# Kernel optimization log

Measured on AMD Instinct MI355X. Metric: run time of the kernel, lower is better.

The kernel has to match this reference:

```python
import jax, jax.numpy as jnp
import numpy as np
from jax.ops import segment_sum, segment_max

N = 38332
E = 1200000
C = 64
POI_LEN = 38333
CAT_LEN = 400
LAYERS = 5


def _glorot(key, shape):
    fan_in, fan_out = shape[0], shape[-1]
    lim = float(np.sqrt(6.0 / (fan_in + fan_out)))
    return jax.random.uniform(key, shape, jnp.float32, -lim, lim)


def gcn_conv(x, src, dst, ew, W, b):
    # PyG GCNConv: x@W, add self-loops (weight 1), symmetric norm, scatter-sum at dst
    h = x @ W  # [N, Cout]
    ar = jnp.arange(N, dtype=src.dtype)
    s = jnp.concatenate([src, ar])
    d = jnp.concatenate([dst, ar])
    w = jnp.concatenate([ew, jnp.ones((N,), ew.dtype)])
    deg = segment_sum(w, d, num_segments=N)
    dinv = jnp.where(deg > 0, jax.lax.rsqrt(jnp.maximum(deg, 1e-12)), 0.0)
    norm = dinv[s] * w * dinv[d]
    out = segment_sum(h[s] * norm[:, None], d, num_segments=N)
    return out + b


def graph_norm(x, w, b, alpha, eps=1e-5):
    mean = jnp.mean(x, axis=0, keepdims=True)
    out = x - alpha * mean
    var = jnp.mean(out * out, axis=0, keepdims=True)
    return out * jax.lax.rsqrt(var + eps) * w + b


def gat_conv(x, src, dst, W, att_src, att_dst, b):
    # PyG GATConv, heads=1, add_self_loops=True, negative_slope=0.2
    h = x @ W  # [N, C]
    ar = jnp.arange(N, dtype=src.dtype)
    s = jnp.concatenate([src, ar])
    d = jnp.concatenate([dst, ar])
    a_s = h @ att_src  # [N]
    a_d = h @ att_dst
    e = jax.nn.leaky_relu(a_s[s] + a_d[d], 0.2)  # [E+N]
    m = segment_max(e, d, num_segments=N)
    ex = jnp.exp(e - m[d])
    z = segment_sum(ex, d, num_segments=N)
    alpha = ex / (z[d] + 1e-16)
    out = segment_sum(h[s] * alpha[:, None], d, num_segments=N)
    return out + b


def setup_inputs() -> dict:
    key = jax.random.key(0)
    ks = jax.random.split(key, 32)
    inp = {
        'poi_idx': jax.random.randint(ks[0], (N,), 0, POI_LEN, jnp.int32),
        'cat_idx': jax.random.randint(ks[1], (N,), 0, CAT_LEN, jnp.int32),
        'feat': jax.random.normal(ks[2], (N, 3), jnp.float32),
        'edge_index': jax.random.randint(ks[3], (2, E), 0, N, jnp.int32),
        'weight': jax.random.uniform(ks[4], (E,), jnp.float32),
        'poi_emb': jax.random.normal(ks[5], (POI_LEN, 300), jnp.float32),
        'cat_emb': jax.random.normal(ks[6], (CAT_LEN, 100), jnp.float32),
        'W_in': _glorot(ks[7], (403, C)),
        'b_in': jnp.zeros((C,), jnp.float32),
        'gcn_W': jax.vmap(lambda k: _glorot(k, (C, C)))(jax.random.split(ks[8], LAYERS)),
        'gcn_b': jnp.zeros((LAYERS, C), jnp.float32),
        'gn_w': jnp.ones((LAYERS, C), jnp.float32),
        'gn_b': jnp.zeros((LAYERS, C), jnp.float32),
        'gn_a': jnp.ones((LAYERS, C), jnp.float32),
        'gat_W': jax.vmap(lambda k: _glorot(k, (C, C)))(jax.random.split(ks[9], LAYERS)),
        'gat_att_src': jax.random.normal(ks[10], (LAYERS, C), jnp.float32) * 0.1,
        'gat_att_dst': jax.random.normal(ks[11], (LAYERS, C), jnp.float32) * 0.1,
        'gat_b': jnp.zeros((LAYERS, C), jnp.float32),
        'W_out': _glorot(ks[12], (C, 1)),
        'b_out': jnp.zeros((1,), jnp.float32),
        'fc1_W': _glorot(ks[13], (N, 128)),
        'fc1_b': jnp.zeros((128,), jnp.float32),
        'fc2_W': _glorot(ks[14], (128, POI_LEN)),
        'fc2_b': jnp.zeros((POI_LEN,), jnp.float32),
    }
    return inp


def reference(poi_idx, cat_idx, feat, edge_index, weight, poi_emb, cat_emb,
              W_in, b_in, gcn_W, gcn_b, gn_w, gn_b, gn_a,
              gat_W, gat_att_src, gat_att_dst, gat_b,
              W_out, b_out, fc1_W, fc1_b, fc2_W, fc2_b):
    src, dst = edge_index[0], edge_index[1]
    lrelu = lambda v: jax.nn.leaky_relu(v, 0.01)  # nn.LeakyReLU default
    x = jnp.concatenate([poi_emb[poi_idx], cat_emb[cat_idx], feat], axis=1)  # [N,403]
    x = lrelu(gcn_conv(x, src, dst, weight, W_in, b_in))  # [N,64]
    for i in range(LAYERS):
        t = gcn_conv(x, src, dst, weight, gcn_W[i], gcn_b[i])
        t = lrelu(graph_norm(t, gn_w[i], gn_b[i], gn_a[i]))
        x = x + t
        t = gat_conv(x, src, dst, gat_W[i], gat_att_src[i], gat_att_dst[i], gat_b[i])
        t = lrelu(graph_norm(t, gn_w[i], gn_b[i], gn_a[i]))
        x = x + t
    x = lrelu(gcn_conv(x, src, dst, weight, W_out, b_out)).reshape(-1)  # [N]
    h = jax.nn.relu(x @ fc1_W + fc1_b)
    out = jax.nn.relu(h @ fc2_W + fc2_b)  # [POI_LEN]
    return out
```

## Files before the change

kernel.cpp:

```cpp
#include <hip/hip_runtime.h>
#include <hip/hip_fp16.h>

#define NN 38332
#define NE 1200000
#define POI 38333
#define NWG 192
#define CHUNK (NE/NWG)
#define SBLK 256
#define FBLK 1024

__device__ __forceinline__ float lrelu01(float v){ return v > 0.f ? v : 0.01f*v; }

__device__ __forceinline__ void load8(const __half* h, int s, int c8, float* f){
  uint4 q = *(const uint4*)((const __half*)h + (size_t)s*64 + c8);
  __half2 h0 = *(__half2*)&q.x, h1 = *(__half2*)&q.y, h2 = *(__half2*)&q.z, h3 = *(__half2*)&q.w;
  float2 r0 = __half22float2(h0), r1 = __half22float2(h1), r2 = __half22float2(h2), r3 = __half22float2(h3);
  f[0]=r0.x; f[1]=r0.y; f[2]=r1.x; f[3]=r1.y; f[4]=r2.x; f[5]=r2.y; f[6]=r3.x; f[7]=r3.y;
}
__device__ __forceinline__ void load8(const float* h, int s, int c8, float* f){
  float4 a = *(const float4*)(h + (size_t)s*64 + c8);
  float4 b = *(const float4*)(h + (size_t)s*64 + c8 + 4);
  f[0]=a.x; f[1]=a.y; f[2]=a.z; f[3]=a.w; f[4]=b.x; f[5]=b.y; f[6]=b.z; f[7]=b.w;
}
__device__ __forceinline__ void store8(float* out, int n, int cb, const float* o){
  *(float4*)&out[(size_t)n*64 + cb]     = make_float4(o[0],o[1],o[2],o[3]);
  *(float4*)&out[(size_t)n*64 + cb + 4] = make_float4(o[4],o[5],o[6],o[7]);
}
__device__ __forceinline__ void store8(__half* out, int n, int cb, const float* o){
  __half2 q0 = __floats2half2_rn(o[0], o[1]);
  __half2 q1 = __floats2half2_rn(o[2], o[3]);
  __half2 q2 = __floats2half2_rn(o[4], o[5]);
  __half2 q3 = __floats2half2_rn(o[6], o[7]);
  uint4 q;
  q.x = *(unsigned*)&q0; q.y = *(unsigned*)&q1; q.z = *(unsigned*)&q2; q.w = *(unsigned*)&q3;
  *(uint4*)((__half*)out + (size_t)n*64 + cb) = q;
}

__global__ __launch_bounds__(1024) void k_hist(const int* __restrict__ dst,
                                               int* __restrict__ partial){
  __shared__ int hist[NN];
  for (int i = threadIdx.x; i < NN; i += 1024) hist[i] = 0;
  __syncthreads();
  int base = blockIdx.x*CHUNK;
  for (int k = threadIdx.x; k < CHUNK; k += 1024)
    atomicAdd(&hist[dst[base + k]], 1);
  __syncthreads();
  for (int i = threadIdx.x; i < NN; i += 1024)
    partial[(size_t)blockIdx.x*NN + i] = hist[i];
}

__global__ __launch_bounds__(256) void k_b1(int* __restrict__ partial, int* __restrict__ counts){
  int bin = blockIdx.x*256 + threadIdx.x;
  if (bin < NN){
    int run = 0;
    for (int wg = 0; wg < NWG; ++wg){
      int v = partial[(size_t)wg*NN + bin];
      partial[(size_t)wg*NN + bin] = run;
      run += v;
    }
    counts[bin] = run;
  }
}

__global__ __launch_bounds__(1024) void k_scan(const int* __restrict__ counts, int* rowptr){
  __shared__ int part[1024];
  int tid = threadIdx.x;
  const int per = (NN + 1023)/1024;
  int base = tid*per;
  int s = 0;
  for (int k = 0; k < per; k++){ int i = base + k; if (i < NN) s += counts[i]; }
  part[tid] = s;
  __syncthreads();
  for (int off = 1; off < 1024; off <<= 1){
    int v = (tid >= off) ? part[tid-off] : 0;
    __syncthreads();
    part[tid] += v;
    __syncthreads();
  }
  int run = (tid == 0) ? 0 : part[tid-1];
  for (int k = 0; k < per; k++){
    int i = base + k;
    if (i < NN){ rowptr[i] = run; run += counts[i]; }
  }
  if (tid == 1023) rowptr[NN] = run;
}

__global__ __launch_bounds__(1024) void k_scatter(const int* __restrict__ src,
                                                  const int* __restrict__ dst,
                                                  const float* __restrict__ ew,
                                                  const int* __restrict__ rowptr,
                                                  const int* __restrict__ partial,
                                                  int2* __restrict__ cw){
  __shared__ int cur[NN];
  for (int i = threadIdx.x; i < NN; i += 1024)
    cur[i] = rowptr[i] + partial[(size_t)blockIdx.x*NN + i];
  __syncthreads();
  int base = blockIdx.x*CHUNK;
  for (int k = threadIdx.x; k < CHUNK; k += 1024){
    int e = base + k;
    int d = dst[e];
    int pos = atomicAdd(&cur[d], 1);
    cw[pos] = make_int2(src[e], __float_as_int(ew[e]));
  }
}

__global__ __launch_bounds__(256) void k_dinv(const int* __restrict__ rowptr,
                                              const int2* __restrict__ cw,
                                              float* __restrict__ dinv){
  int lane = threadIdx.x & 63;
  int n = blockIdx.x*4 + (threadIdx.x >> 6);
  int beg = rowptr[n], end = rowptr[n+1];
  float s = 0.f;
  for (int e = beg + lane; e < end; e += 64) s += __int_as_float(cw[e].y);
  #pragma unroll
  for (int off = 32; off; off >>= 1) s += __shfl_xor(s, off);
  if (lane == 0) dinv[n] = rsqrtf(1.0f + s);
}

__global__ __launch_bounds__(256) void k_scale(const int* __restrict__ rowptr,
                                               const float* __restrict__ dinv,
                                               int2* __restrict__ cw){
  int lane = threadIdx.x & 63;
  int n = blockIdx.x*4 + (threadIdx.x >> 6);
  float dn = dinv[n];
  int beg = rowptr[n], end = rowptr[n+1];
  for (int e = beg + lane; e < end; e += 64){
    int2 p = cw[e];
    cw[e].y = __float_as_int(dinv[p.x]*__int_as_float(p.y)*dn);
  }
}

template<int K>
__global__ __launch_bounds__(256) void k_proj(const float* __restrict__ emb,
                                              const float* __restrict__ W,
                                              float* __restrict__ outp, int rows){
  int lane = threadIdx.x & 63;
  int base = __builtin_amdgcn_readfirstlane(blockIdx.x*16 + (threadIdx.x >> 6)*4);
  float acc[4] = {0.f,0.f,0.f,0.f};
  constexpr int NCH = (K + 63)/64;
  #pragma unroll
  for (int ch = 0; ch < NCH; ++ch){
    float Wreg[64];
    #pragma unroll
    for (int j = 0; j < 64; ++j)
      Wreg[j] = (ch*64 + j < K) ? W[(ch*64 + j)*64 + lane] : 0.f;
    #pragma unroll
    for (int r = 0; r < 4; ++r){
      int row = base + r;
      if (row < rows){
        const float* er = emb + (size_t)row*K + ch*64;
        #pragma unroll
        for (int j = 0; j < 64; ++j)
          if (ch*64 + j < K) acc[r] = fmaf(er[j], Wreg[j], acc[r]);
      }
    }
  }
  #pragma unroll
  for (int r = 0; r < 4; ++r){
    int row = base + r;
    if (row < rows) outp[(size_t)row*64 + lane] = acc[r];
  }
}

__global__ __launch_bounds__(256) void k_gather(const int* __restrict__ poi_idx,
                                                const int* __restrict__ cat_idx,
                                                const float* __restrict__ feat,
                                                const float* __restrict__ pproj,
                                                const float* __restrict__ cproj,
                                                const float* __restrict__ Wf,
                                                __half* __restrict__ outh){
  int i = blockIdx.x*256 + threadIdx.x;
  int n = i >> 6, c = i & 63;
  float f0 = feat[n*3], f1 = feat[n*3+1], f2 = feat[n*3+2];
  float v = pproj[(size_t)poi_idx[n]*64 + c] + cproj[(size_t)cat_idx[n]*64 + c];
  v = fmaf(f0, Wf[c], v);
  v = fmaf(f1, Wf[64 + c], v);
  v = fmaf(f2, Wf[128 + c], v);
  outh[i] = __float2half(v);
}

template<bool ATT, bool RESID>
__global__ __launch_bounds__(256) void k_lin64f(float* __restrict__ x,
                                                const __half* __restrict__ t,
                                                const float* __restrict__ stats,
                                                const float* __restrict__ gb,
                                                const float* __restrict__ W,
                                                const float* __restrict__ att_src,
                                                const float* __restrict__ att_dst,
                                                __half* __restrict__ h,
                                                float* __restrict__ a_s,
                                                float* __restrict__ a_d){
  int lane = threadIdx.x & 63;
  int base = blockIdx.x*32 + (threadIdx.x >> 6)*8;
  float Wreg[64];
  #pragma unroll
  for (int j = 0; j < 64; ++j) Wreg[j] = W[j*64 + lane];
  float coef = 0.f, shift = 0.f, gbv = 0.f;
  if (RESID){
    coef  = stats[128 + lane];
    shift = stats[192 + lane];
    gbv   = gb[lane];
  }
  float as_l = 0.f, ad_l = 0.f;
  if (ATT){ as_l = att_src[lane]; ad_l = att_dst[lane]; }
  #pragma unroll
  for (int r = 0; r < 8; ++r){
    int row = base + r;
    if (row < NN){
      float xn = x[(size_t)row*64 + lane];
      if (RESID){
        float tv = __half2float(t[(size_t)row*64 + lane]);
        xn += lrelu01((tv - shift)*coef + gbv);
        x[(size_t)row*64 + lane] = xn;
      }
      int xi = __float_as_int(xn);
      float acc = 0.f;
      #pragma unroll
      for (int j = 0; j < 64; ++j)
        acc = fmaf(__int_as_float(__builtin_amdgcn_readlane(xi, j)), Wreg[j], acc);
      h[(size_t)row*64 + lane] = __float2half(acc);
      if (ATT){
        float s1 = acc*as_l, s2 = acc*ad_l;
        #pragma unroll
        for (int off = 32; off; off >>= 1){ s1 += __shfl_xor(s1, off); s2 += __shfl_xor(s2, off); }
        if (lane == 0){ a_s[row] = s1; a_d[row] = s2; }
      }
    }
  }
}

template<bool DO_LRELU, typename TIN, typename TOUT>
__global__ __launch_bounds__(256) void k_gcn_prop(const TIN* __restrict__ h,
                                                  const int* __restrict__ rowptr,
                                                  const int2* __restrict__ cw,
                                                  const float* __restrict__ dinv,
                                                  const float* __restrict__ bias,
                                                  TOUT* __restrict__ out){
  int lane = threadIdx.x & 63;
  int n = __builtin_amdgcn_readfirstlane(blockIdx.x*4 + (threadIdx.x >> 6));
  int beg = rowptr[n], end = rowptr[n+1];
  int deg = end - beg;
  int g  = lane >> 3;
  int c8 = (lane & 7) << 3;
  float acc[8] = {0.f,0.f,0.f,0.f,0.f,0.f,0.f,0.f};
  float acc2[8] = {0.f,0.f,0.f,0.f,0.f,0.f,0.f,0.f};
  if (deg < 64){
    int sv = n; float wv = 0.f;
    if (lane < deg){
      int2 p = cw[beg + lane];
      sv = p.x; wv = __int_as_float(p.y);
    } else if (lane == deg){
      float di = dinv[n];
      wv = di*di;
    }
    int ne = deg + 1;
    int nit = (ne + 15) >> 4;
    float wA0 = __shfl(wv, g),     wB0 = __shfl(wv, 8 + g);
    int   sA0 = __shfl(sv, g),     sB0 = __shfl(sv, 8 + g);
    float fA0[8], fB0[8];
    load8(h, sA0, c8, fA0); load8(h, sB0, c8, fB0);
    for (int it = 1; it < nit; ++it){
      int eiA = (it << 4) + g, eiB = eiA + 8;
      float wA1 = __shfl(wv, eiA), wB1 = __shfl(wv, eiB);
      int   sA1 = __shfl(sv, eiA), sB1 = __shfl(sv, eiB);
      float fA1[8], fB1[8];
      load8(h, sA1, c8, fA1); load8(h, sB1, c8, fB1);
      #pragma unroll
      for (int j = 0; j < 8; ++j){
        acc[j]  = fmaf(wA0, fA0[j], acc[j]);
        acc2[j] = fmaf(wB0, fB0[j], acc2[j]);
      }
      wA0 = wA1; wB0 = wB1;
      #pragma unroll
      for (int j = 0; j < 8; ++j){ fA0[j] = fA1[j]; fB0[j] = fB1[j]; }
    }
    #pragma unroll
    for (int j = 0; j < 8; ++j){
      acc[j]  = fmaf(wA0, fA0[j], acc[j]);
      acc2[j] = fmaf(wB0, fB0[j], acc2[j]);
    }
  } else {
    {
      float di = dinv[n];
      float w = (g == 0) ? di*di : 0.f;
      float f[8]; load8(h, n, c8, f);
      #pragma unroll
      for (int j = 0; j < 8; ++j) acc[j] = fmaf(w, f[j], acc[j]);
    }
    int nit = (deg + 7) >> 3;
    for (int it = 0; it < nit; ++it){
      int ei = (it << 3) + g;
      int2 p = cw[beg + (ei < deg ? ei : 0)];
      float w = (ei < deg) ? __int_as_float(p.y) : 0.f;
      float f[8]; load8(h, p.x, c8, f);
      #pragma unroll
      for (int j = 0; j < 8; ++j) acc[j] = fmaf(w, f[j], acc[j]);
    }
  }
  #pragma unroll
  for (int j = 0; j < 8; ++j) acc[j] += acc2[j];
  #pragma unroll
  for (int m = 8; m < 64; m <<= 1){
    #pragma unroll
    for (int j = 0; j < 8; ++j) acc[j] += __shfl_xor(acc[j], m);
  }
  if (lane < 8){
    int cb = lane << 3;
    float4 b0 = *(const float4*)&bias[cb];
    float4 b1 = *(const float4*)&bias[cb + 4];
    float o[8] = {acc[0]+b0.x, acc[1]+b0.y, acc[2]+b0.z, acc[3]+b0.w,
                  acc[4]+b1.x, acc[5]+b1.y, acc[6]+b1.z, acc[7]+b1.w};
    if (DO_LRELU){
      #pragma unroll
      for (int j = 0; j < 8; ++j) o[j] = lrelu01(o[j]);
    }
    store8(out, n, cb, o);
  }
}

__global__ __launch_bounds__(256) void k_gat_prop(const __half* __restrict__ h,
                                                  const int* __restrict__ rowptr,
                                                  const int2* __restrict__ cw,
                                                  const float* __restrict__ a_s,
                                                  const float* __restrict__ a_d,
                                                  const float* __restrict__ bias,
                                                  __half* __restrict__ out){
  int lane = threadIdx.x & 63;
  int n = __builtin_amdgcn_readfirstlane(blockIdx.x*4 + (threadIdx.x >> 6));
  int beg = rowptr[n], end = rowptr[n+1];
  int deg = end - beg;
  float ad = a_d[n];
  float se = a_s[n] + ad; se = se > 0.f ? se : 0.2f*se;
  if (deg <= 64){
    int s = 0; float v = -1e30f;
    if (lane < deg){
      s = cw[beg + lane].x;
      v = a_s[s] + ad; v = v > 0.f ? v : 0.2f*v;
    }
    float m = fmaxf(se, v);
    #pragma unroll
    for (int off = 32; off; off >>= 1) m = fmaxf(m, __shfl_xor(m, off));
    float ev = (lane < deg) ? __expf(v - m) : 0.f;
    float z = ev;
    #pragma unroll
    for (int off = 32; off; off >>= 1) z += __shfl_xor(z, off);
    float es = __expf(se - m);
    z += es;
    float zinv = 1.0f/(z + 1e-16f);
    int g = lane >> 3, c8 = (lane & 7) << 3;
    float acc[8] = {0.f,0.f,0.f,0.f,0.f,0.f,0.f,0.f};
    float acc2[8] = {0.f,0.f,0.f,0.f,0.f,0.f,0.f,0.f};
    { float f[8]; load8(h, n, c8, f);
      float w = (g == 0) ? es : 0.f;
      #pragma unroll
      for (int j = 0; j < 8; ++j) acc[j] = fmaf(w, f[j], acc[j]);
    }
    int nit = (deg + 15) >> 4;
    if (nit > 0){
      float wA0 = __shfl(ev, g),     wB0 = __shfl(ev, 8 + g);
      int   sA0 = __shfl(s,  g),     sB0 = __shfl(s,  8 + g);
      float fA0[8], fB0[8];
      load8(h, sA0, c8, fA0); load8(h, sB0, c8, fB0);
      for (int it = 1; it < nit; ++it){
        int eiA = (it << 4) + g, eiB = eiA + 8;
        float wA1 = __shfl(ev, eiA), wB1 = __shfl(ev, eiB);
        int   sA1 = __shfl(s,  eiA), sB1 = __shfl(s,  eiB);
        float fA1[8], fB1[8];
        load8(h, sA1, c8, fA1); load8(h, sB1, c8, fB1);
        #pragma unroll
        for (int j = 0; j < 8; ++j){
          acc[j]  = fmaf(wA0, fA0[j], acc[j]);
          acc2[j] = fmaf(wB0, fB0[j], acc2[j]);
        }
        wA0 = wA1; wB0 = wB1;
        #pragma unroll
        for (int j = 0; j < 8; ++j){ fA0[j] = fA1[j]; fB0[j] = fB1[j]; }
      }
      #pragma unroll
      for (int j = 0; j < 8; ++j){
        acc[j]  = fmaf(wA0, fA0[j], acc[j]);
        acc2[j] = fmaf(wB0, fB0[j], acc2[j]);
      }
    }
    #pragma unroll
    for (int j = 0; j < 8; ++j) acc[j] += acc2[j];
    #pragma unroll
    for (int mm = 8; mm < 64; mm <<= 1){
      #pragma unroll
      for (int j = 0; j < 8; ++j) acc[j] += __shfl_xor(acc[j], mm);
    }
    if (lane < 8){
      int cb = lane << 3;
      float4 b0 = *(const float4*)&bias[cb];
      float4 b1 = *(const float4*)&bias[cb + 4];
      float o[8] = {fmaf(acc[0],zinv,b0.x), fmaf(acc[1],zinv,b0.y), fmaf(acc[2],zinv,b0.z), fmaf(acc[3],zinv,b0.w),
                    fmaf(acc[4],zinv,b1.x), fmaf(acc[5],zinv,b1.y), fmaf(acc[6],zinv,b1.z), fmaf(acc[7],zinv,b1.w)};
      store8(out, n, cb, o);
    }
  } else {
    float m = se;
    for (int e = beg + lane; e < end; e += 64){
      float v = a_s[cw[e].x] + ad; v = v > 0.f ? v : 0.2f*v;
      m = fmaxf(m, v);
    }
    #pragma unroll
    for (int off = 32; off; off >>= 1) m = fmaxf(m, __shfl_xor(m, off));
    float z = 0.f;
    for (int e = beg + lane; e < end; e += 64){
      float v = a_s[cw[e].x] + ad; v = v > 0.f ? v : 0.2f*v;
      z += __expf(v - m);
    }
    #pragma unroll
    for (int off = 32; off; off >>= 1) z += __shfl_xor(z, off);
    float es = __expf(se - m);
    z += es;
    float zinv = 1.0f/(z + 1e-16f);
    float acc = es*(float)h[(size_t)n*64 + lane];
    for (int e = beg; e < end; ++e){
      int sj = cw[e].x;
      float v = a_s[sj] + ad; v = v > 0.f ? v : 0.2f*v;
      acc = fmaf(__expf(v - m), (float)h[(size_t)sj*64 + lane], acc);
    }
    out[(size_t)n*64 + lane] = __float2half(acc*zinv + bias[lane]);
  }
}

__global__ __launch_bounds__(256) void k_colstats(const __half* __restrict__ t,
                                                  float* __restrict__ pstats){
  int c4  = (threadIdx.x & 15)*4;
  int sub = threadIdx.x >> 4;
  float s0=0.f,s1=0.f,s2=0.f,s3=0.f, q0=0.f,q1=0.f,q2=0.f,q3=0.f;
  for (int n = blockIdx.x*16 + sub; n < NN; n += gridDim.x*16){
    uint2 u = *(const uint2*)((const __half*)t + (size_t)n*64 + c4);
    __half2 h0 = *(__half2*)&u.x, h1 = *(__half2*)&u.y;
    float2 r0 = __half22float2(h0), r1 = __half22float2(h1);
    s0 += r0.x; q0 = fmaf(r0.x, r0.x, q0);
    s1 += r0.y; q1 = fmaf(r0.y, r0.y, q1);
    s2 += r1.x; q2 = fmaf(r1.x, r1.x, q2);
    s3 += r1.y; q3 = fmaf(r1.y, r1.y, q3);
  }
  __shared__ float ls[256][4], ls2[256][4];
  ls[threadIdx.x][0]=s0; ls[threadIdx.x][1]=s1; ls[threadIdx.x][2]=s2; ls[threadIdx.x][3]=s3;
  ls2[threadIdx.x][0]=q0; ls2[threadIdx.x][1]=q1; ls2[threadIdx.x][2]=q2; ls2[threadIdx.x][3]=q3;
  __syncthreads();
  if (threadIdx.x < 16){
    int cg = threadIdx.x;
    float a0=0.f,a1=0.f,a2=0.f,a3=0.f, b0=0.f,b1=0.f,b2=0.f,b3=0.f;
    #pragma unroll
    for (int k = 0; k < 16; ++k){
      int idx = k*16 + cg;
      a0 += ls[idx][0]; a1 += ls[idx][1]; a2 += ls[idx][2]; a3 += ls[idx][3];
      b0 += ls2[idx][0]; b1 += ls2[idx][1]; b2 += ls2[idx][2]; b3 += ls2[idx][3];
    }
    int cb = cg*4;
    pstats[blockIdx.x*128 + cb    ] = a0;
    pstats[blockIdx.x*128 + cb + 1] = a1;
    pstats[blockIdx.x*128 + cb + 2] = a2;
    pstats[blockIdx.x*128 + cb + 3] = a3;
    pstats[blockIdx.x*128 + 64 + cb    ] = b0;
    pstats[blockIdx.x*128 + 64 + cb + 1] = b1;
    pstats[blockIdx.x*128 + 64 + cb + 2] = b2;
    pstats[blockIdx.x*128 + 64 + cb + 3] = b3;
  }
}

__global__ __launch_bounds__(256) void k_chan(const float* __restrict__ pstats,
                                              const float* __restrict__ gw,
                                              const float* __restrict__ ga,
                                              float* __restrict__ stats){
  int lane = threadIdx.x & 63, w = threadIdx.x >> 6;
  float s = 0.f, s2 = 0.f;
  for (int blk = w*(SBLK/4); blk < (w+1)*(SBLK/4); ++blk){
    s  += pstats[blk*128 + lane];
    s2 += pstats[blk*128 + 64 + lane];
  }
  __shared__ float ls[256], ls2[256];
  ls[threadIdx.x] = s; ls2[threadIdx.x] = s2;
  __syncthreads();
  if (threadIdx.x < 64){
    int c = threadIdx.x;
    s  = ls[c]  + ls[c+64]  + ls[c+128]  + ls[c+192];
    s2 = ls2[c] + ls2[c+64] + ls2[c+128] + ls2[c+192];
    const float invN = 1.0f/(float)NN;
    float m  = s*invN, ms = s2*invN, a = ga[c];
    float var = ms - m*m*a*(2.0f - a);
    stats[128 + c] = rsqrtf(var + 1e-5f)*gw[c];
    stats[192 + c] = a*m;
  }
}

__global__ __launch_bounds__(256) void k_outlinf(const float* __restrict__ x,
                                                 const __half* __restrict__ t,
                                                 const float* __restrict__ stats,
                                                 const float* __restrict__ gb,
                                                 const float* __restrict__ Wout,
                                                 float* __restrict__ h1){
  int lane = threadIdx.x & 63, wave = threadIdx.x >> 6;
  int n = blockIdx.x*4 + wave;
  float coef  = stats[128 + lane];
  float shift = stats[192 + lane];
  float xn = x[(size_t)n*64 + lane];
  float tv = __half2float(t[(size_t)n*64 + lane]);
  xn += lrelu01((tv - shift)*coef + gb[lane]);
  float v = xn*Wout[lane];
  #pragma unroll
  for (int off = 32; off; off >>= 1) v += __shfl_xor(v, off);
  if (lane == 0) h1[n] = v;
}

__global__ __launch_bounds__(256) void k_prop1(const float* __restrict__ h1,
                                               const int* __restrict__ rowptr,
                                               const int2* __restrict__ cw,
                                               const float* __restrict__ dinv,
                                               const float* __restrict__ b_out,
                                               float* __restrict__ xs){
  int lane = threadIdx.x & 63;
  int n = blockIdx.x*32 + (threadIdx.x >> 6)*8 + (lane >> 3);
  bool ok = n < NN;
  int beg = ok ? rowptr[n] : 0;
  int end = ok ? rowptr[n+1] : 0;
  float acc = 0.f;
  for (int e = beg + (lane & 7); e < end; e += 8){
    int2 p = cw[e];
    acc = fmaf(__int_as_float(p.y), h1[p.x], acc);
  }
  acc += __shfl_xor(acc, 1);
  acc += __shfl_xor(acc, 2);
  acc += __shfl_xor(acc, 4);
  if (ok && (lane & 7) == 0){
    float di = dinv[n];
    xs[n] = lrelu01(acc + di*di*h1[n] + b_out[0]);
  }
}

__global__ __launch_bounds__(256) void k_fc1(const float* __restrict__ xs,
                                             const float* __restrict__ W,
                                             float* __restrict__ pfc){
  int j = threadIdx.x & 127, half = threadIdx.x >> 7;
  float acc = 0.f;
  for (int n = blockIdx.x*2 + half; n < NN; n += gridDim.x*2)
    acc = fmaf(xs[n], W[(size_t)n*128 + j], acc);
  __shared__ float ls[256];
  ls[threadIdx.x] = acc;
  __syncthreads();
  if (threadIdx.x < 128) pfc[blockIdx.x*128 + j] = ls[j] + ls[128 + j];
}

__global__ __launch_bounds__(256) void k_fcr(const float* __restrict__ pfc,
                                             const float* __restrict__ fc1_b,
                                             float* __restrict__ hfc){
  int j = blockIdx.x;
  int tid = threadIdx.x;
  float acc = 0.f;
  #pragma unroll
  for (int k = 0; k < FBLK/256; ++k)
    acc += pfc[(size_t)(tid + k*256)*128 + j];
  __shared__ float ls[256];
  ls[tid] = acc;
  __syncthreads();
  for (int off = 128; off > 0; off >>= 1){
    if (tid < off) ls[tid] += ls[tid + off];
    __syncthreads();
  }
  if (tid == 0){
    float v = ls[0] + fc1_b[j];
    hfc[j] = v > 0.f ? v : 0.f;
  }
}

__global__ __launch_bounds__(256) void k_fc2(const float* __restrict__ hfc,
                                             const float* __restrict__ W2,
                                             const float* __restrict__ b2,
                                             float* __restrict__ out){
  __shared__ float hs[128];
  if (threadIdx.x < 128) hs[threadIdx.x] = hfc[threadIdx.x];
  __syncthreads();
  int p = blockIdx.x*64 + (threadIdx.x >> 2);
  int q = threadIdx.x & 3;
  if (p < POI){
    float acc = 0.f;
    #pragma unroll
    for (int j = q; j < 128; j += 4)
      acc = fmaf(hs[j], W2[(size_t)j*POI + p], acc);
    acc += __shfl_xor(acc, 1);
    acc += __shfl_xor(acc, 2);
    if (q == 0){
      float v = acc + b2[p];
      out[p] = v > 0.f ? v : 0.f;
    }
  }
}

extern "C" void kernel_launch(void* const* d_in, const int* in_sizes, int n_in,
                              void* d_out, int out_size, void* d_ws, size_t ws_size,
                              hipStream_t stream) {
  const int*   poi_idx = (const int*)d_in[0];
  const int*   cat_idx = (const int*)d_in[1];
  const float* feat    = (const float*)d_in[2];
  const int*   eidx    = (const int*)d_in[3];
  const int*   src     = eidx;
  const int*   dst     = eidx + NE;
  const float* ew      = (const float*)d_in[4];
  const float* poi_emb = (const float*)d_in[5];
  const float* cat_emb = (const float*)d_in[6];
  const float* W_in    = (const float*)d_in[7];
  const float* b_in    = (const float*)d_in[8];
  const float* gcn_W   = (const float*)d_in[9];
  const float* gcn_b   = (const float*)d_in[10];
  const float* gn_w    = (const float*)d_in[11];
  const float* gn_b    = (const float*)d_in[12];
  const float* gn_a    = (const float*)d_in[13];
  const float* gat_W   = (const float*)d_in[14];
  const float* att_s   = (const float*)d_in[15];
  const float* att_d   = (const float*)d_in[16];
  const float* gat_b   = (const float*)d_in[17];
  const float* W_out   = (const float*)d_in[18];
  const float* b_out   = (const float*)d_in[19];
  const float* fc1_W   = (const float*)d_in[20];
  const float* fc1_b   = (const float*)d_in[21];
  const float* fc2_W   = (const float*)d_in[22];
  const float* fc2_b   = (const float*)d_in[23];
  float* out = (float*)d_out;

  char* p = (char*)d_ws;
  auto alloc = [&](size_t bytes){ void* r = (void*)p; p += (bytes + 255) & ~(size_t)255; return r; };
  float*  x      = (float*) alloc((size_t)NN*64*4);
  __half* t      = (__half*)alloc((size_t)NN*64*2);
  __half* h      = (__half*)alloc((size_t)NN*64*2);
  int*    partial= (int*)   alloc((size_t)NWG*NN*4);
  float*  pproj  = (float*) partial;
  float*  cproj  = (float*) alloc((size_t)400*64*4);
  int2*   cw     = (int2*)  alloc((size_t)NE*8);
  float*  dinv   = (float*) alloc(NN*4);
  int*    counts = (int*)   alloc(NN*4);
  int*    rowptr = (int*)   alloc((NN+1)*4);
  float*  a_s    = (float*) alloc(NN*4);
  float*  a_d    = (float*) alloc(NN*4);
  float*  pstats = (float*) alloc((size_t)SBLK*128*4);
  float*  stats  = (float*) alloc(256*4);
  float*  h1     = (float*) alloc(NN*4);
  float*  xs     = (float*) alloc(NN*4);
  float*  pfc    = (float*) alloc((size_t)FBLK*128*4);
  float*  hfc    = (float*) alloc(128*4);

  const int G_N   = (NN + 255)/256;
  const int G_W4  = NN/4;
  const int G_L   = (NN + 31)/32;
  const int G_PJ  = (POI + 15)/16;
  const int G_EL  = NN*64/256;
  const int G_P1  = (NN + 31)/32;
  const int G_F2  = (POI + 63)/64;

  k_hist   <<<NWG, 1024, 0, stream>>>(dst, partial);
  k_b1     <<<G_N, 256, 0, stream>>>(partial, counts);
  k_scan   <<<1, 1024, 0, stream>>>(counts, rowptr);
  k_scatter<<<NWG, 1024, 0, stream>>>(src, dst, ew, rowptr, partial, cw);
  k_dinv   <<<G_W4, 256, 0, stream>>>(rowptr, cw, dinv);
  k_scale  <<<G_W4, 256, 0, stream>>>(rowptr, dinv, cw);

  k_proj<300><<<G_PJ, 256, 0, stream>>>(poi_emb, W_in, pproj, POI);
  k_proj<100><<<25, 256, 0, stream>>>(cat_emb, W_in + 300*64, cproj, 400);
  k_gather<<<G_EL, 256, 0, stream>>>(poi_idx, cat_idx, feat, pproj, cproj, W_in + 400*64, t);
  k_gcn_prop<true, __half, float><<<G_W4, 256, 0, stream>>>(t, rowptr, cw, dinv, b_in, x);

  for (int i = 0; i < 5; i++){
    if (i == 0)
      k_lin64f<false,false><<<G_L, 256, 0, stream>>>(x, nullptr, nullptr, nullptr,
                                                     gcn_W, nullptr, nullptr, h, nullptr, nullptr);
    else
      k_lin64f<false,true><<<G_L, 256, 0, stream>>>(x, t, stats, gn_b + (i-1)*64,
                                                    gcn_W + i*4096, nullptr, nullptr, h, nullptr, nullptr);
    k_gcn_prop<false, __half, __half><<<G_W4, 256, 0, stream>>>(h, rowptr, cw, dinv, gcn_b + i*64, t);
    k_colstats<<<SBLK, 256, 0, stream>>>(t, pstats);
    k_chan<<<1, 256, 0, stream>>>(pstats, gn_w + i*64, gn_a + i*64, stats);
    k_lin64f<true,true><<<G_L, 256, 0, stream>>>(x, t, stats, gn_b + i*64,
                                                 gat_W + i*4096, att_s + i*64, att_d + i*64, h, a_s, a_d);
    k_gat_prop<<<G_W4, 256, 0, stream>>>(h, rowptr, cw, a_s, a_d, gat_b + i*64, t);
    k_colstats<<<SBLK, 256, 0, stream>>>(t, pstats);
    k_chan<<<1, 256, 0, stream>>>(pstats, gn_w + i*64, gn_a + i*64, stats);
  }

  k_outlinf<<<G_W4, 256, 0, stream>>>(x, t, stats, gn_b + 4*64, W_out, h1);
  k_prop1<<<G_P1, 256, 0, stream>>>(h1, rowptr, cw, dinv, b_out, xs);
  k_fc1<<<FBLK, 256, 0, stream>>>(xs, fc1_W, pfc);
  k_fcr<<<128, 256, 0, stream>>>(pfc, fc1_b, hfc);
  k_fc2<<<G_F2, 256, 0, stream>>>(hfc, fc2_W, fc2_b, out);
}
```

Before: 896.1 us.

## Split propagation kernels across channel halves and shrink histogram partials to 16-bit

The GCN and GAT propagation kernels now launch twice as many blocks, and each wave handles one 32-channel half of a node. This gives 16 edges in flight per iteration, and the short-degree path becomes a fixed 2–4 gather step with no loop. The per-workgroup histogram partials are stored as unsigned short, halving that buffer's traffic in the CSR build. The trade-off is that the edge indices, softmax weights and attention logits for each node are loaded and computed twice. The 16-bit partials are safe only while per-bin counts stay below 65536.

```diff
diff --git a/kernel.cpp b/kernel.cpp
--- a/kernel.cpp
+++ b/kernel.cpp
@@ -37,7 +37,7 @@
 }
 
 __global__ __launch_bounds__(1024) void k_hist(const int* __restrict__ dst,
-                                               int* __restrict__ partial){
+                                               unsigned short* __restrict__ partial){
   __shared__ int hist[NN];
   for (int i = threadIdx.x; i < NN; i += 1024) hist[i] = 0;
   __syncthreads();
@@ -46,16 +46,17 @@
     atomicAdd(&hist[dst[base + k]], 1);
   __syncthreads();
   for (int i = threadIdx.x; i < NN; i += 1024)
-    partial[(size_t)blockIdx.x*NN + i] = hist[i];
-}
-
-__global__ __launch_bounds__(256) void k_b1(int* __restrict__ partial, int* __restrict__ counts){
+    partial[(size_t)blockIdx.x*NN + i] = (unsigned short)hist[i];
+}
+
+__global__ __launch_bounds__(256) void k_b1(unsigned short* __restrict__ partial,
+                                            int* __restrict__ counts){
   int bin = blockIdx.x*256 + threadIdx.x;
   if (bin < NN){
     int run = 0;
     for (int wg = 0; wg < NWG; ++wg){
       int v = partial[(size_t)wg*NN + bin];
-      partial[(size_t)wg*NN + bin] = run;
+      partial[(size_t)wg*NN + bin] = (unsigned short)run;
       run += v;
     }
     counts[bin] = run;
@@ -89,11 +90,11 @@
                                                   const int* __restrict__ dst,
                                                   const float* __restrict__ ew,
                                                   const int* __restrict__ rowptr,
-                                                  const int* __restrict__ partial,
+                                                  const unsigned short* __restrict__ partial,
                                                   int2* __restrict__ cw){
   __shared__ int cur[NN];
   for (int i = threadIdx.x; i < NN; i += 1024)
-    cur[i] = rowptr[i] + partial[(size_t)blockIdx.x*NN + i];
+    cur[i] = rowptr[i] + (int)partial[(size_t)blockIdx.x*NN + i];
   __syncthreads();
   int base = blockIdx.x*CHUNK;
   for (int k = threadIdx.x; k < CHUNK; k += 1024){
@@ -237,13 +238,13 @@
                                                   const float* __restrict__ bias,
                                                   TOUT* __restrict__ out){
   int lane = threadIdx.x & 63;
-  int n = __builtin_amdgcn_readfirstlane(blockIdx.x*4 + (threadIdx.x >> 6));
+  int half = blockIdx.x & 1;
+  int n = __builtin_amdgcn_readfirstlane((blockIdx.x >> 1)*4 + (threadIdx.x >> 6));
   int beg = rowptr[n], end = rowptr[n+1];
   int deg = end - beg;
-  int g  = lane >> 3;
-  int c8 = (lane & 7) << 3;
+  int g  = lane >> 2;
+  int co = half*32 + (lane & 3)*8;
   float acc[8] = {0.f,0.f,0.f,0.f,0.f,0.f,0.f,0.f};
-  float acc2[8] = {0.f,0.f,0.f,0.f,0.f,0.f,0.f,0.f};
   if (deg < 64){
     int sv = n; float wv = 0.f;
     if (lane < deg){
@@ -254,58 +255,51 @@
       wv = di*di;
     }
     int ne = deg + 1;
-    int nit = (ne + 15) >> 4;
-    float wA0 = __shfl(wv, g),     wB0 = __shfl(wv, 8 + g);
-    int   sA0 = __shfl(sv, g),     sB0 = __shfl(sv, 8 + g);
-    float fA0[8], fB0[8];
-    load8(h, sA0, c8, fA0); load8(h, sB0, c8, fB0);
-    for (int it = 1; it < nit; ++it){
-      int eiA = (it << 4) + g, eiB = eiA + 8;
-      float wA1 = __shfl(wv, eiA), wB1 = __shfl(wv, eiB);
-      int   sA1 = __shfl(sv, eiA), sB1 = __shfl(sv, eiB);
-      float fA1[8], fB1[8];
-      load8(h, sA1, c8, fA1); load8(h, sB1, c8, fB1);
+    float w0 = __shfl(wv, g),      w1 = __shfl(wv, 16 + g);
+    int   s0 = __shfl(sv, g),      s1 = __shfl(sv, 16 + g);
+    float f0[8], f1[8];
+    load8(h, s0, co, f0); load8(h, s1, co, f1);
+    if (ne > 32){
+      float w2 = __shfl(wv, 32 + g), w3 = __shfl(wv, 48 + g);
+      int   s2 = __shfl(sv, 32 + g), s3 = __shfl(sv, 48 + g);
+      float f2[8], f3[8];
+      load8(h, s2, co, f2); load8(h, s3, co, f3);
       #pragma unroll
       for (int j = 0; j < 8; ++j){
-        acc[j]  = fmaf(wA0, fA0[j], acc[j]);
-        acc2[j] = fmaf(wB0, fB0[j], acc2[j]);
+        acc[j] = fmaf(w2, f2[j], acc[j]);
+        acc[j] = fmaf(w3, f3[j], acc[j]);
       }
-      wA0 = wA1; wB0 = wB1;
-      #pragma unroll
-      for (int j = 0; j < 8; ++j){ fA0[j] = fA1[j]; fB0[j] = fB1[j]; }
     }
     #pragma unroll
     for (int j = 0; j < 8; ++j){
-      acc[j]  = fmaf(wA0, fA0[j], acc[j]);
-      acc2[j] = fmaf(wB0, fB0[j], acc2[j]);
+      acc[j] = fmaf(w0, f0[j], acc[j]);
+      acc[j] = fmaf(w1, f1[j], acc[j]);
     }
   } else {
     {
       float di = dinv[n];
       float w = (g == 0) ? di*di : 0.f;
-      float f[8]; load8(h, n, c8, f);
+      float f[8]; load8(h, n, co, f);
       #pragma unroll
       for (int j = 0; j < 8; ++j) acc[j] = fmaf(w, f[j], acc[j]);
     }
-    int nit = (deg + 7) >> 3;
+    int nit = (deg + 15) >> 4;
     for (int it = 0; it < nit; ++it){
-      int ei = (it << 3) + g;
+      int ei = (it << 4) + g;
       int2 p = cw[beg + (ei < deg ? ei : 0)];
       float w = (ei < deg) ? __int_as_float(p.y) : 0.f;
-      float f[8]; load8(h, p.x, c8, f);
+      float f[8]; load8(h, p.x, co, f);
       #pragma unroll
       for (int j = 0; j < 8; ++j) acc[j] = fmaf(w, f[j], acc[j]);
     }
   }
   #pragma unroll
-  for (int j = 0; j < 8; ++j) acc[j] += acc2[j];
-  #pragma unroll
-  for (int m = 8; m < 64; m <<= 1){
+  for (int m = 4; m < 64; m <<= 1){
     #pragma unroll
     for (int j = 0; j < 8; ++j) acc[j] += __shfl_xor(acc[j], m);
   }
-  if (lane < 8){
-    int cb = lane << 3;
+  if (lane < 4){
+    int cb = half*32 + lane*8;
     float4 b0 = *(const float4*)&bias[cb];
     float4 b1 = *(const float4*)&bias[cb + 4];
     float o[8] = {acc[0]+b0.x, acc[1]+b0.y, acc[2]+b0.z, acc[3]+b0.w,
@@ -326,71 +320,59 @@
                                                   const float* __restrict__ bias,
                                                   __half* __restrict__ out){
   int lane = threadIdx.x & 63;
-  int n = __builtin_amdgcn_readfirstlane(blockIdx.x*4 + (threadIdx.x >> 6));
+  int half = blockIdx.x & 1;
+  int n = __builtin_amdgcn_readfirstlane((blockIdx.x >> 1)*4 + (threadIdx.x >> 6));
   int beg = rowptr[n], end = rowptr[n+1];
   int deg = end - beg;
   float ad = a_d[n];
   float se = a_s[n] + ad; se = se > 0.f ? se : 0.2f*se;
-  if (deg <= 64){
-    int s = 0; float v = -1e30f;
+  if (deg < 64){
+    int s = n; float v = -1e30f;
     if (lane < deg){
       s = cw[beg + lane].x;
       v = a_s[s] + ad; v = v > 0.f ? v : 0.2f*v;
-    }
-    float m = fmaxf(se, v);
+    } else if (lane == deg){
+      v = se;
+    }
+    float m = v;
     #pragma unroll
     for (int off = 32; off; off >>= 1) m = fmaxf(m, __shfl_xor(m, off));
-    float ev = (lane < deg) ? __expf(v - m) : 0.f;
+    float ev = (lane <= deg) ? __expf(v - m) : 0.f;
     float z = ev;
     #pragma unroll
     for (int off = 32; off; off >>= 1) z += __shfl_xor(z, off);
-    float es = __expf(se - m);
-    z += es;
     float zinv = 1.0f/(z + 1e-16f);
-    int g = lane >> 3, c8 = (lane & 7) << 3;
+    int g = lane >> 2;
+    int co = half*32 + (lane & 3)*8;
     float acc[8] = {0.f,0.f,0.f,0.f,0.f,0.f,0.f,0.f};
-    float acc2[8] = {0.f,0.f,0.f,0.f,0.f,0.f,0.f,0.f};
-    { float f[8]; load8(h, n, c8, f);
-      float w = (g == 0) ? es : 0.f;
-      #pragma unroll
-      for (int j = 0; j < 8; ++j) acc[j] = fmaf(w, f[j], acc[j]);
-    }
-    int nit = (deg + 15) >> 4;
-    if (nit > 0){
-      float wA0 = __shfl(ev, g),     wB0 = __shfl(ev, 8 + g);
-      int   sA0 = __shfl(s,  g),     sB0 = __shfl(s,  8 + g);
-      float fA0[8], fB0[8];
-      load8(h, sA0, c8, fA0); load8(h, sB0, c8, fB0);
-      for (int it = 1; it < nit; ++it){
-        int eiA = (it << 4) + g, eiB = eiA + 8;
-        float wA1 = __shfl(ev, eiA), wB1 = __shfl(ev, eiB);
-        int   sA1 = __shfl(s,  eiA), sB1 = __shfl(s,  eiB);
-        float fA1[8], fB1[8];
-        load8(h, sA1, c8, fA1); load8(h, sB1, c8, fB1);
-        #pragma unroll
-        for (int j = 0; j < 8; ++j){
-          acc[j]  = fmaf(wA0, fA0[j], acc[j]);
-          acc2[j] = fmaf(wB0, fB0[j], acc2[j]);
-        }
-        wA0 = wA1; wB0 = wB1;
-        #pragma unroll
-        for (int j = 0; j < 8; ++j){ fA0[j] = fA1[j]; fB0[j] = fB1[j]; }
-      }
+    int ne = deg + 1;
+    float w0 = __shfl(ev, g),      w1 = __shfl(ev, 16 + g);
+    int   s0 = __shfl(s, g),       s1 = __shfl(s, 16 + g);
+    float f0[8], f1[8];
+    load8(h, s0, co, f0); load8(h, s1, co, f1);
+    if (ne > 32){
+      float w2 = __shfl(ev, 32 + g), w3 = __shfl(ev, 48 + g);
+      int   s2 = __shfl(s, 32 + g),  s3 = __shfl(s, 48 + g);
+      float f2[8], f3[8];
+      load8(h, s2, co, f2); load8(h, s3, co, f3);
       #pragma unroll
       for (int j = 0; j < 8; ++j){
-        acc[j]  = fmaf(wA0, fA0[j], acc[j]);
-        acc2[j] = fmaf(wB0, fB0[j], acc2[j]);
+        acc[j] = fmaf(w2, f2[j], acc[j]);
+        acc[j] = fmaf(w3, f3[j], acc[j]);
       }
     }
     #pragma unroll
-    for (int j = 0; j < 8; ++j) acc[j] += acc2[j];
-    #pragma unroll
-    for (int mm = 8; mm < 64; mm <<= 1){
+    for (int j = 0; j < 8; ++j){
+      acc[j] = fmaf(w0, f0[j], acc[j]);
+      acc[j] = fmaf(w1, f1[j], acc[j]);
+    }
+    #pragma unroll
+    for (int mm = 4; mm < 64; mm <<= 1){
       #pragma unroll
       for (int j = 0; j < 8; ++j) acc[j] += __shfl_xor(acc[j], mm);
     }
-    if (lane < 8){
-      int cb = lane << 3;
+    if (lane < 4){
+      int cb = half*32 + lane*8;
       float4 b0 = *(const float4*)&bias[cb];
       float4 b1 = *(const float4*)&bias[cb + 4];
       float o[8] = {fmaf(acc[0],zinv,b0.x), fmaf(acc[1],zinv,b0.y), fmaf(acc[2],zinv,b0.z), fmaf(acc[3],zinv,b0.w),
@@ -415,13 +397,15 @@
     float es = __expf(se - m);
     z += es;
     float zinv = 1.0f/(z + 1e-16f);
-    float acc = es*(float)h[(size_t)n*64 + lane];
+    int c = half*32 + (lane & 31);
+    float acc = (lane < 32) ? es*(float)h[(size_t)n*64 + c] : 0.f;
     for (int e = beg; e < end; ++e){
       int sj = cw[e].x;
       float v = a_s[sj] + ad; v = v > 0.f ? v : 0.2f*v;
-      acc = fmaf(__expf(v - m), (float)h[(size_t)sj*64 + lane], acc);
-    }
-    out[(size_t)n*64 + lane] = __float2half(acc*zinv + bias[lane]);
+      float w = __expf(v - m);
+      if (lane < 32) acc = fmaf(w, (float)h[(size_t)sj*64 + c], acc);
+    }
+    if (lane < 32) out[(size_t)n*64 + c] = __float2half(acc*zinv + bias[c]);
   }
 }
 
@@ -627,7 +611,7 @@
   float*  x      = (float*) alloc((size_t)NN*64*4);
   __half* t      = (__half*)alloc((size_t)NN*64*2);
   __half* h      = (__half*)alloc((size_t)NN*64*2);
-  int*    partial= (int*)   alloc((size_t)NWG*NN*4);
+  unsigned short* partial = (unsigned short*)alloc((size_t)NWG*NN*2);
   float*  pproj  = (float*) partial;
   float*  cproj  = (float*) alloc((size_t)400*64*4);
   int2*   cw     = (int2*)  alloc((size_t)NE*8);
@@ -645,6 +629,7 @@
 
   const int G_N   = (NN + 255)/256;
   const int G_W4  = NN/4;
+  const int G_PS  = 2*(NN/4);
   const int G_L   = (NN + 31)/32;
   const int G_PJ  = (POI + 15)/16;
   const int G_EL  = NN*64/256;
@@ -661,7 +646,7 @@
   k_proj<300><<<G_PJ, 256, 0, stream>>>(poi_emb, W_in, pproj, POI);
   k_proj<100><<<25, 256, 0, stream>>>(cat_emb, W_in + 300*64, cproj, 400);
   k_gather<<<G_EL, 256, 0, stream>>>(poi_idx, cat_idx, feat, pproj, cproj, W_in + 400*64, t);
-  k_gcn_prop<true, __half, float><<<G_W4, 256, 0, stream>>>(t, rowptr, cw, dinv, b_in, x);
+  k_gcn_prop<true, __half, float><<<G_PS, 256, 0, stream>>>(t, rowptr, cw, dinv, b_in, x);
 
   for (int i = 0; i < 5; i++){
     if (i == 0)
@@ -670,12 +655,12 @@
     else
       k_lin64f<false,true><<<G_L, 256, 0, stream>>>(x, t, stats, gn_b + (i-1)*64,
                                                     gcn_W + i*4096, nullptr, nullptr, h, nullptr, nullptr);
-    k_gcn_prop<false, __half, __half><<<G_W4, 256, 0, stream>>>(h, rowptr, cw, dinv, gcn_b + i*64, t);
+    k_gcn_prop<false, __half, __half><<<G_PS, 256, 0, stream>>>(h, rowptr, cw, dinv, gcn_b + i*64, t);
     k_colstats<<<SBLK, 256, 0, stream>>>(t, pstats);
     k_chan<<<1, 256, 0, stream>>>(pstats, gn_w + i*64, gn_a + i*64, stats);
     k_lin64f<true,true><<<G_L, 256, 0, stream>>>(x, t, stats, gn_b + i*64,
                                                  gat_W + i*4096, att_s + i*64, att_d + i*64, h, a_s, a_d);
-    k_gat_prop<<<G_W4, 256, 0, stream>>>(h, rowptr, cw, a_s, a_d, gat_b + i*64, t);
+    k_gat_prop<<<G_PS, 256, 0, stream>>>(h, rowptr, cw, a_s, a_d, gat_b + i*64, t);
     k_colstats<<<SBLK, 256, 0, stream>>>(t, pstats);
     k_chan<<<1, 256, 0, stream>>>(pstats, gn_w + i*64, gn_a + i*64, stats);
   }
```

New measurement: 1.054 ms. +17.6%, slower.
